# Kernel optimization log

Hardware: AMD Instinct MI355X
Metric: run time of the kernel (lower is better)

## Reference

```python
import jax, jax.numpy as jnp
import numpy as np

V = 256   # ascii_max_dim / output vocab
H = 1024  # h_size


def _lstm(x1h, W_ih, W_hh, b_ih, b_hh):
    """Single-layer unidirectional LSTM (PyTorch gate order i,f,g,o).
    x1h: [B,T,V] one-hot inputs; returns hidden states [B,T,H]."""
    B, T, _ = x1h.shape
    # input projection for all timesteps at once: [B,T,4H]
    xg = jnp.einsum('btv,gv->btg', x1h, W_ih) + b_ih + b_hh

    def step(carry, xt):
        h, c = carry
        gates = xt + h @ W_hh.T  # [B,4H]
        i, f, g, o = jnp.split(gates, 4, axis=-1)
        i = jax.nn.sigmoid(i)
        f = jax.nn.sigmoid(f)
        g = jnp.tanh(g)
        o = jax.nn.sigmoid(o)
        c = f * c + i * g
        h = o * jnp.tanh(c)
        return (h, c), h

    h0 = jnp.zeros((B, H), xg.dtype)
    c0 = jnp.zeros((B, H), xg.dtype)
    _, hs = jax.lax.scan(step, (h0, c0), jnp.swapaxes(xg, 0, 1))  # [T,B,H]
    return jnp.swapaxes(hs, 0, 1)  # [B,T,H]


def setup_inputs() -> dict:
    key = jax.random.key(0)
    ks = jax.random.split(key, 8)
    B, T = 8, 2048
    s = 0.05
    return {
        'Xs': jax.random.randint(ks[0], (B, T), 0, V),
        'ys': jax.random.randint(ks[1], (B, T), 0, V),
        'predict': 0,
        'W_ih': jax.random.normal(ks[2], (4 * H, V), dtype=jnp.float32) * s,
        'W_hh': jax.random.normal(ks[3], (4 * H, H), dtype=jnp.float32) * s,
        'b_ih': jax.random.normal(ks[4], (4 * H,), dtype=jnp.float32) * s,
        'b_hh': jax.random.normal(ks[5], (4 * H,), dtype=jnp.float32) * s,
        'W1': jax.random.normal(ks[6], (V, H), dtype=jnp.float32) * s,
        'b1': jax.random.normal(ks[7], (V,), dtype=jnp.float32) * s,
    }


def reference(Xs, ys, predict, W_ih, W_hh, b_ih, b_hh, W1, b1):
    # one-hot encode char ids -> [B,T,V]
    x1h = jax.nn.one_hot(Xs, V, dtype=W_ih.dtype)
    hs = _lstm(x1h, W_ih, W_hh, b_ih, b_hh)            # [B,T,H]
    logits = jnp.einsum('bth,vh->btv', hs, W1) + b1    # [B,T,V]
    if predict:
        prob = jax.nn.softmax(logits, axis=-1)
        return prob, jnp.argmax(prob, axis=-1)
    # CrossEntropyLoss (mean over timesteps) per sequence, averaged over sequences;
    # with equal lengths this is the mean NLL over all (B,T) positions.
    logp = jax.nn.log_softmax(logits, axis=-1)
    nll = -jnp.take_along_axis(logp, ys[..., None], axis=-1).squeeze(-1)
    return jnp.mean(nll)
```

## Files before the change

kernel.cpp:

```cpp
#include <hip/hip_runtime.h>

#define H_  1024
#define B_  8
#define T_  2048
#define V_  256
#define NWG 256
#define NTH 512
#define WPS (B_ * H_ / 4)

typedef unsigned long long u64;

__device__ __forceinline__ u64 agload64(const u64* p) {
  return __hip_atomic_load(p, __ATOMIC_RELAXED, __HIP_MEMORY_SCOPE_AGENT);
}
__device__ __forceinline__ void agstore64(u64* p, u64 v) {
  __hip_atomic_store(p, v, __ATOMIC_RELAXED, __HIP_MEMORY_SCOPE_AGENT);
}
__device__ __forceinline__ unsigned f2bf(float f) {
  unsigned u = __builtin_bit_cast(unsigned, f);
  return (u + 0x7fffu + ((u >> 16) & 1u)) >> 16;
}
__device__ __forceinline__ unsigned f2bf14(float f) {
  unsigned u = __builtin_bit_cast(unsigned, f);
  return ((u + 0x1FFFFu + ((u >> 18) & 1u)) >> 18) << 2;
}

__global__ __launch_bounds__(NTH, 1)
void charrnn_lstm(const int* __restrict__ Xs, const int* __restrict__ ys,
                  const float* __restrict__ W_ih, const float* __restrict__ W_hh,
                  const float* __restrict__ b_ih, const float* __restrict__ b_hh,
                  const float* __restrict__ W1, const float* __restrict__ b1,
                  float* __restrict__ out, u64* __restrict__ hg64)
{
  __shared__ float hstage[B_][H_];
  __shared__ float Wis[16][V_];
  __shared__ float stash[H_];
  __shared__ float logits_s[V_];
  __shared__ float gates_s[16][8];
  __shared__ float c_s[4][8];
  __shared__ float bias_s[16];
  __shared__ int   xw[8][32];

  const int wg   = blockIdx.x;
  const int tid  = threadIdx.x;
  const int b_g  = wg & 7;
  const int slot = wg >> 3;
  const int row  = tid >> 5;
  const int seg  = tid & 31;

  const int rg = (row >> 2) * H_ + wg * 4 + (row & 3);
  float4 wreg[8];
  #pragma unroll
  for (int q = 0; q < 8; ++q)
    wreg[q] = *(const float4*)&W_hh[(size_t)rg * H_ + seg * 4 + q * 128];

  for (int i = tid; i < 16 * (V_ / 4); i += NTH) {
    int rl = i >> 6;
    int kq = i & 63;
    int rr = (rl >> 2) * H_ + wg * 4 + (rl & 3);
    *(float4*)&Wis[rl][kq * 4] = *(const float4*)&W_ih[(size_t)rr * V_ + kq * 4];
  }
  if (tid < 16) {
    int rr = (tid >> 2) * H_ + wg * 4 + (tid & 3);
    bias_s[tid] = b_ih[rr] + b_hh[rr];
  }
  if (tid < 32) c_s[tid >> 3][tid & 7] = 0.f;

  int   pending = 0, chunk = 0, ptau = 0;
  float wg_loss = 0.f;

  auto do_chunk = [&]() {
    const int v_loc = tid >> 6, lane64 = tid & 63;
    const int vg = chunk * 8 + v_loc;
    const float* wrow = &W1[(size_t)vg * H_];
    float4 la = make_float4(0.f, 0.f, 0.f, 0.f);
    #pragma unroll
    for (int j = 0; j < 4; ++j) {
      const int k0 = lane64 * 4 + j * 256;
      const float4 w4 = *(const float4*)&wrow[k0];
      const float4 h4 = *(const float4*)&stash[k0];
      la.x = fmaf(w4.x, h4.x, la.x);
      la.y = fmaf(w4.y, h4.y, la.y);
      la.z = fmaf(w4.z, h4.z, la.z);
      la.w = fmaf(w4.w, h4.w, la.w);
    }
    float l = (la.x + la.y) + (la.z + la.w);
    #pragma unroll
    for (int m = 1; m < 64; m <<= 1) l += __shfl_xor(l, m, 64);
    if (lane64 == 0) logits_s[vg] = l + b1[vg];
    chunk++;
    if (chunk == 32) {
      __syncthreads();
      if (tid < 64) {
        float mx = -3.4e38f;
        #pragma unroll
        for (int i2 = 0; i2 < 4; ++i2) mx = fmaxf(mx, logits_s[tid * 4 + i2]);
        #pragma unroll
        for (int m = 1; m < 64; m <<= 1) mx = fmaxf(mx, __shfl_xor(mx, m, 64));
        float se = 0.f;
        #pragma unroll
        for (int i2 = 0; i2 < 4; ++i2) se += __expf(logits_s[tid * 4 + i2] - mx);
        #pragma unroll
        for (int m = 1; m < 64; m <<= 1) se += __shfl_xor(se, m, 64);
        if (tid == 0) {
          const float ly = logits_s[ys[b_g * T_ + ptau]];
          wg_loss += -(ly - mx - __logf(se));
        }
      }
      pending = 0;
      chunk = 0;
      __syncthreads();
    }
  };

  __syncthreads();

  for (int t = 0; t < T_; ++t) {
    const u64* hb = hg64 + (size_t)((t + 1) & 1) * WPS;
    const unsigned tagp = (unsigned)t & 3u;
    u64 v[4];
    for (;;) {
      bool ok = true;
      #pragma unroll
      for (int i = 0; i < 4; ++i) v[i] = agload64(&hb[i * NTH + tid]);
      #pragma unroll
      for (int i = 0; i < 4; ++i) ok &= (((unsigned)v[i] & 3u) == tagp);
      if (ok) break;
      __builtin_amdgcn_s_sleep(1);
    }
    #pragma unroll
    for (int i = 0; i < 4; ++i) {
      const int idx = i * NTH + tid;
      const int b = idx >> 8, u4 = idx & 255;
      const unsigned lo = (unsigned)v[i], hi = (unsigned)(v[i] >> 32);
      float4 f;
      f.x = __builtin_bit_cast(float, (lo & 0xFFFCu) << 16);
      f.y = __builtin_bit_cast(float, lo & 0xFFFF0000u);
      f.z = __builtin_bit_cast(float, (hi & 0xFFFFu) << 16);
      f.w = __builtin_bit_cast(float, hi & 0xFFFF0000u);
      *(float4*)&hstage[b][u4 * 4] = f;
    }
    if ((t & 31) == 0 && tid < 256) {
      const int b = tid >> 5, tt = t + (tid & 31);
      xw[b][tid & 31] = (tt < T_) ? Xs[b * T_ + tt] : 0;
    }
    __syncthreads();

    float4 acc[8];
    #pragma unroll
    for (int b = 0; b < 8; ++b) acc[b] = make_float4(0.f, 0.f, 0.f, 0.f);
    #pragma unroll
    for (int q = 0; q < 8; ++q) {
      const int k0 = seg * 4 + q * 128;
      const float4 w = wreg[q];
      #pragma unroll
      for (int b = 0; b < 8; ++b) {
        const float4 h4 = *(const float4*)&hstage[b][k0];
        acc[b].x = fmaf(w.x, h4.x, acc[b].x);
        acc[b].y = fmaf(w.y, h4.y, acc[b].y);
        acc[b].z = fmaf(w.z, h4.z, acc[b].z);
        acc[b].w = fmaf(w.w, h4.w, acc[b].w);
      }
    }
    float s[8];
    #pragma unroll
    for (int b = 0; b < 8; ++b) s[b] = (acc[b].x + acc[b].y) + (acc[b].z + acc[b].w);
    #pragma unroll
    for (int m = 1; m < 32; m <<= 1) {
      #pragma unroll
      for (int b = 0; b < 8; ++b) s[b] += __shfl_xor(s[b], m, 64);
    }
    if (seg < 8)
      gates_s[row][seg] = s[seg] + Wis[row][xw[seg][t & 31]] + bias_s[row];
    __syncthreads();

    if (tid < 32) {
      const int jj = tid >> 3, b = tid & 7;
      float iv = gates_s[jj][b],      fv = gates_s[4 + jj][b];
      float gv = gates_s[8 + jj][b],  ov = gates_s[12 + jj][b];
      iv = 1.f / (1.f + __expf(-iv));
      fv = 1.f / (1.f + __expf(-fv));
      gv = tanhf(gv);
      ov = 1.f / (1.f + __expf(-ov));
      const float c = fv * c_s[jj][b] + iv * gv;
      c_s[jj][b] = c;
      const float h = ov * tanhf(c);
      const unsigned full = f2bf(h);
      const unsigned tagd = f2bf14(h) | ((unsigned)(t + 1) & 3u);
      const unsigned r16 = (jj == 0) ? tagd : full;
      const unsigned p1 = (unsigned)__shfl((int)r16, b + 8, 64);
      const unsigned p2 = (unsigned)__shfl((int)r16, b + 16, 64);
      const unsigned p3 = (unsigned)__shfl((int)r16, b + 24, 64);
      if (tid < 8) {
        const u64 w = (u64)r16 | ((u64)p1 << 16) | ((u64)p2 << 32) | ((u64)p3 << 48);
        agstore64(&hg64[(size_t)(t & 1) * WPS + tid * 256 + wg], w);
      }
    }

    const int tau = t - 1;
    const bool newst = (tau >= 0 && (tau & 31) == slot && !pending);
    if (newst) {
      for (int i = tid; i < H_; i += NTH) stash[i] = hstage[b_g][i];
    }
    if (newst) { pending = 1; chunk = 0; ptau = tau; }
    __syncthreads();

    if (pending) do_chunk();
  }

  while (pending) do_chunk();

  if (slot == 31) {
    const u64* hb = hg64 + (size_t)((T_ - 1) & 1) * WPS;
    if (tid < 256) {
      u64 w;
      do { w = agload64(&hb[b_g * 256 + tid]); }
      while (((unsigned)w & 3u) != ((unsigned)T_ & 3u));
      const unsigned lo = (unsigned)w, hi = (unsigned)(w >> 32);
      float4 f;
      f.x = __builtin_bit_cast(float, (lo & 0xFFFCu) << 16);
      f.y = __builtin_bit_cast(float, lo & 0xFFFF0000u);
      f.z = __builtin_bit_cast(float, (hi & 0xFFFFu) << 16);
      f.w = __builtin_bit_cast(float, hi & 0xFFFF0000u);
      *(float4*)&stash[tid * 4] = f;
    }
    pending = 1; chunk = 0; ptau = T_ - 1;
    __syncthreads();
    while (pending) do_chunk();
  }

  if (tid == 0) atomicAdd(out, wg_loss * (1.0f / (B_ * T_)));
}

extern "C" void kernel_launch(void* const* d_in, const int* in_sizes, int n_in,
                              void* d_out, int out_size, void* d_ws, size_t ws_size,
                              hipStream_t stream) {
  const int*   Xs   = (const int*)d_in[0];
  const int*   ys   = (const int*)d_in[1];
  const float* W_ih = (const float*)d_in[3];
  const float* W_hh = (const float*)d_in[4];
  const float* b_ih = (const float*)d_in[5];
  const float* b_hh = (const float*)d_in[6];
  const float* W1   = (const float*)d_in[7];
  const float* b1   = (const float*)d_in[8];
  float* out = (float*)d_out;

  u64* hg64 = (u64*)d_ws;

  hipMemsetAsync(d_out, 0, sizeof(float) * (size_t)out_size, stream);
  hipMemsetAsync(d_ws, 0, 2 * WPS * sizeof(u64), stream);

  void* args[] = { (void*)&Xs, (void*)&ys, (void*)&W_ih, (void*)&W_hh,
                   (void*)&b_ih, (void*)&b_hh, (void*)&W1, (void*)&b1,
                   (void*)&out, (void*)&hg64 };
  hipError_t e = hipLaunchCooperativeKernel((const void*)charrnn_lstm, dim3(NWG),
                                            dim3(NTH), args, 0, stream);
  if (e != hipSuccess) {
    hipLaunchKernelGGL(charrnn_lstm, dim3(NWG), dim3(NTH), 0, stream,
                       Xs, ys, W_ih, W_hh, b_ih, b_hh, W1, b1, out, hg64);
  }
}
```

Baseline: 8.746 ms.

## Partition LSTM by batch element with per-group sync and bf16 register weights

Each workgroup now owns one batch element and 32 hidden units (128 gate rows) instead of 4 units across all batch elements. Each group of 32 workgroups exchanges hidden state through its own small buffer, so every step polls only 256 words. The recurrent weights are packed as bf16 pairs into 128 registers per thread, and the input projection is gathered per step from W_ih instead of being staged in shared memory. The aim is less global polling and synchronisation fan-in per step, at the cost of reduced weight precision and heavy register pressure under launch_bounds(512,2), which may cause spills.

```diff
diff --git a/kernel.cpp b/kernel.cpp
--- a/kernel.cpp
+++ b/kernel.cpp
@@ -6,9 +6,12 @@
 #define V_  256
 #define NWG 256
 #define NTH 512
-#define WPS (B_ * H_ / 4)
+#define NGRP 8
+#define NRANK 32
+#define WPG 256
 
 typedef unsigned long long u64;
+typedef unsigned u32;
 
 __device__ __forceinline__ u64 agload64(const u64* p) {
   return __hip_atomic_load(p, __ATOMIC_RELAXED, __HIP_MEMORY_SCOPE_AGENT);
@@ -16,55 +19,58 @@
 __device__ __forceinline__ void agstore64(u64* p, u64 v) {
   __hip_atomic_store(p, v, __ATOMIC_RELAXED, __HIP_MEMORY_SCOPE_AGENT);
 }
-__device__ __forceinline__ unsigned f2bf(float f) {
-  unsigned u = __builtin_bit_cast(unsigned, f);
+__device__ __forceinline__ u32 f2bf(float f) {
+  u32 u = __builtin_bit_cast(u32, f);
   return (u + 0x7fffu + ((u >> 16) & 1u)) >> 16;
 }
-__device__ __forceinline__ unsigned f2bf14(float f) {
-  unsigned u = __builtin_bit_cast(unsigned, f);
+__device__ __forceinline__ u32 f2bf14(float f) {
+  u32 u = __builtin_bit_cast(u32, f);
   return ((u + 0x1FFFFu + ((u >> 18) & 1u)) >> 18) << 2;
 }
-
-__global__ __launch_bounds__(NTH, 1)
+__device__ __forceinline__ float bflo(u32 w) {
+  return __builtin_bit_cast(float, w << 16);
+}
+__device__ __forceinline__ float bfhi(u32 w) {
+  return __builtin_bit_cast(float, w & 0xFFFF0000u);
+}
+
+__global__ __launch_bounds__(NTH, 2)
 void charrnn_lstm(const int* __restrict__ Xs, const int* __restrict__ ys,
                   const float* __restrict__ W_ih, const float* __restrict__ W_hh,
                   const float* __restrict__ b_ih, const float* __restrict__ b_hh,
                   const float* __restrict__ W1, const float* __restrict__ b1,
                   float* __restrict__ out, u64* __restrict__ hg64)
 {
-  __shared__ float hstage[B_][H_];
-  __shared__ float Wis[16][V_];
+  __shared__ float hstage[4 * 264];
   __shared__ float stash[H_];
   __shared__ float logits_s[V_];
-  __shared__ float gates_s[16][8];
-  __shared__ float c_s[4][8];
-  __shared__ float bias_s[16];
-  __shared__ int   xw[8][32];
+  __shared__ float gates_s[128];
+  __shared__ float c_s[NRANK];
 
   const int wg   = blockIdx.x;
   const int tid  = threadIdx.x;
-  const int b_g  = wg & 7;
-  const int slot = wg >> 3;
-  const int row  = tid >> 5;
-  const int seg  = tid & 31;
-
-  const int rg = (row >> 2) * H_ + wg * 4 + (row & 3);
-  float4 wreg[8];
+  const int g    = wg & 7;
+  const int rank = wg >> 3;
+  const int slot = rank;
+  const int r_loc = tid >> 2;
+  const int seg   = tid & 3;
+  const int g4    = r_loc >> 5;
+  const int u_loc = r_loc & 31;
+  const int rg    = g4 * H_ + rank * NRANK + u_loc;
+
+  u64* gbuf = hg64 + (size_t)g * (2 * WPG);
+
+  u32 wp[128];
   #pragma unroll
-  for (int q = 0; q < 8; ++q)
-    wreg[q] = *(const float4*)&W_hh[(size_t)rg * H_ + seg * 4 + q * 128];
-
-  for (int i = tid; i < 16 * (V_ / 4); i += NTH) {
-    int rl = i >> 6;
-    int kq = i & 63;
-    int rr = (rl >> 2) * H_ + wg * 4 + (rl & 3);
-    *(float4*)&Wis[rl][kq * 4] = *(const float4*)&W_ih[(size_t)rr * V_ + kq * 4];
-  }
-  if (tid < 16) {
-    int rr = (tid >> 2) * H_ + wg * 4 + (tid & 3);
-    bias_s[tid] = b_ih[rr] + b_hh[rr];
-  }
-  if (tid < 32) c_s[tid >> 3][tid & 7] = 0.f;
+  for (int q = 0; q < 64; ++q) {
+    const float4 w4 = *(const float4*)&W_hh[(size_t)rg * H_ + seg * 256 + q * 4];
+    wp[2 * q]     = f2bf(w4.x) | (f2bf(w4.y) << 16);
+    wp[2 * q + 1] = f2bf(w4.z) | (f2bf(w4.w) << 16);
+  }
+  const float breg = b_ih[rg] + b_hh[rg];
+  if (tid < NRANK) c_s[tid] = 0.f;
+
+  float xv = W_ih[(size_t)rg * V_ + Xs[g * T_]];
 
   int   pending = 0, chunk = 0, ptau = 0;
   float wg_loss = 0.f;
@@ -103,7 +109,7 @@
         #pragma unroll
         for (int m = 1; m < 64; m <<= 1) se += __shfl_xor(se, m, 64);
         if (tid == 0) {
-          const float ly = logits_s[ys[b_g * T_ + ptau]];
+          const float ly = logits_s[ys[g * T_ + ptau]];
           wg_loss += -(ly - mx - __logf(se));
         }
       }
@@ -116,91 +122,71 @@
   __syncthreads();
 
   for (int t = 0; t < T_; ++t) {
-    const u64* hb = hg64 + (size_t)((t + 1) & 1) * WPS;
-    const unsigned tagp = (unsigned)t & 3u;
-    u64 v[4];
-    for (;;) {
-      bool ok = true;
-      #pragma unroll
-      for (int i = 0; i < 4; ++i) v[i] = agload64(&hb[i * NTH + tid]);
-      #pragma unroll
-      for (int i = 0; i < 4; ++i) ok &= (((unsigned)v[i] & 3u) == tagp);
-      if (ok) break;
-      __builtin_amdgcn_s_sleep(1);
-    }
-    #pragma unroll
-    for (int i = 0; i < 4; ++i) {
-      const int idx = i * NTH + tid;
-      const int b = idx >> 8, u4 = idx & 255;
-      const unsigned lo = (unsigned)v[i], hi = (unsigned)(v[i] >> 32);
+    const u64* hb = gbuf + ((t + 1) & 1) * WPG;
+    const u32 tagp = (u32)t & 3u;
+    if (tid < WPG) {
+      u64 v;
+      do { v = agload64(&hb[tid]); } while (((u32)v & 3u) != tagp);
+      const u32 lo = (u32)v, hi = (u32)(v >> 32);
       float4 f;
       f.x = __builtin_bit_cast(float, (lo & 0xFFFCu) << 16);
       f.y = __builtin_bit_cast(float, lo & 0xFFFF0000u);
       f.z = __builtin_bit_cast(float, (hi & 0xFFFFu) << 16);
       f.w = __builtin_bit_cast(float, hi & 0xFFFF0000u);
-      *(float4*)&hstage[b][u4 * 4] = f;
-    }
-    if ((t & 31) == 0 && tid < 256) {
-      const int b = tid >> 5, tt = t + (tid & 31);
-      xw[b][tid & 31] = (tt < T_) ? Xs[b * T_ + tt] : 0;
-    }
-    __syncthreads();
-
-    float4 acc[8];
+      *(float4*)&hstage[(tid >> 6) * 264 + ((4 * tid) & 255)] = f;
+    }
+    const int cnext = Xs[g * T_ + ((t + 1 < T_) ? t + 1 : T_ - 1)];
+    const float xv_next = W_ih[(size_t)rg * V_ + cnext];
+    __syncthreads();
+
+    const float* hseg = &hstage[seg * 264];
+    float a0 = 0.f, a1 = 0.f;
     #pragma unroll
-    for (int b = 0; b < 8; ++b) acc[b] = make_float4(0.f, 0.f, 0.f, 0.f);
-    #pragma unroll
-    for (int q = 0; q < 8; ++q) {
-      const int k0 = seg * 4 + q * 128;
-      const float4 w = wreg[q];
-      #pragma unroll
-      for (int b = 0; b < 8; ++b) {
-        const float4 h4 = *(const float4*)&hstage[b][k0];
-        acc[b].x = fmaf(w.x, h4.x, acc[b].x);
-        acc[b].y = fmaf(w.y, h4.y, acc[b].y);
-        acc[b].z = fmaf(w.z, h4.z, acc[b].z);
-        acc[b].w = fmaf(w.w, h4.w, acc[b].w);
-      }
-    }
-    float s[8];
-    #pragma unroll
-    for (int b = 0; b < 8; ++b) s[b] = (acc[b].x + acc[b].y) + (acc[b].z + acc[b].w);
-    #pragma unroll
-    for (int m = 1; m < 32; m <<= 1) {
-      #pragma unroll
-      for (int b = 0; b < 8; ++b) s[b] += __shfl_xor(s[b], m, 64);
-    }
-    if (seg < 8)
-      gates_s[row][seg] = s[seg] + Wis[row][xw[seg][t & 31]] + bias_s[row];
-    __syncthreads();
-
-    if (tid < 32) {
-      const int jj = tid >> 3, b = tid & 7;
-      float iv = gates_s[jj][b],      fv = gates_s[4 + jj][b];
-      float gv = gates_s[8 + jj][b],  ov = gates_s[12 + jj][b];
+    for (int q = 0; q < 64; ++q) {
+      const float4 h4 = *(const float4*)&hseg[q * 4];
+      const u32 wa = wp[2 * q], wb = wp[2 * q + 1];
+      a0 = fmaf(bflo(wa), h4.x, a0);
+      a1 = fmaf(bfhi(wa), h4.y, a1);
+      a0 = fmaf(bflo(wb), h4.z, a0);
+      a1 = fmaf(bfhi(wb), h4.w, a1);
+    }
+    float p = a0 + a1;
+    p += __shfl_xor(p, 1, 64);
+    p += __shfl_xor(p, 2, 64);
+    if (seg == 0) gates_s[r_loc] = p + xv + breg;
+    __syncthreads();
+
+    if (tid < NRANK) {
+      const int u = tid;
+      float iv = gates_s[u],      fv = gates_s[32 + u];
+      float gv = gates_s[64 + u], ov = gates_s[96 + u];
       iv = 1.f / (1.f + __expf(-iv));
       fv = 1.f / (1.f + __expf(-fv));
       gv = tanhf(gv);
       ov = 1.f / (1.f + __expf(-ov));
-      const float c = fv * c_s[jj][b] + iv * gv;
-      c_s[jj][b] = c;
+      const float c = fv * c_s[u] + iv * gv;
+      c_s[u] = c;
       const float h = ov * tanhf(c);
-      const unsigned full = f2bf(h);
-      const unsigned tagd = f2bf14(h) | ((unsigned)(t + 1) & 3u);
-      const unsigned r16 = (jj == 0) ? tagd : full;
-      const unsigned p1 = (unsigned)__shfl((int)r16, b + 8, 64);
-      const unsigned p2 = (unsigned)__shfl((int)r16, b + 16, 64);
-      const unsigned p3 = (unsigned)__shfl((int)r16, b + 24, 64);
+      const u32 full = f2bf(h);
+      const u32 tagd = f2bf14(h) | ((u32)(t + 1) & 3u);
+      const u32 r16 = ((u & 3) == 0) ? tagd : full;
+      const u32 v0 = (u32)__shfl((int)r16, 4 * tid,     64);
+      const u32 v1 = (u32)__shfl((int)r16, 4 * tid + 1, 64);
+      const u32 v2 = (u32)__shfl((int)r16, 4 * tid + 2, 64);
+      const u32 v3 = (u32)__shfl((int)r16, 4 * tid + 3, 64);
       if (tid < 8) {
-        const u64 w = (u64)r16 | ((u64)p1 << 16) | ((u64)p2 << 32) | ((u64)p3 << 48);
-        agstore64(&hg64[(size_t)(t & 1) * WPS + tid * 256 + wg], w);
+        const u64 w = (u64)v0 | ((u64)v1 << 16) | ((u64)v2 << 32) | ((u64)v3 << 48);
+        agstore64(&gbuf[(t & 1) * WPG + rank * 8 + tid], w);
       }
     }
+    xv = xv_next;
 
     const int tau = t - 1;
     const bool newst = (tau >= 0 && (tau & 31) == slot && !pending);
     if (newst) {
-      for (int i = tid; i < H_; i += NTH) stash[i] = hstage[b_g][i];
+      const int i0 = tid, i1 = tid + 512;
+      stash[i0] = hstage[(i0 >> 8) * 264 + (i0 & 255)];
+      stash[i1] = hstage[(i1 >> 8) * 264 + (i1 & 255)];
     }
     if (newst) { pending = 1; chunk = 0; ptau = tau; }
     __syncthreads();
@@ -211,18 +197,17 @@
   while (pending) do_chunk();
 
   if (slot == 31) {
-    const u64* hb = hg64 + (size_t)((T_ - 1) & 1) * WPS;
-    if (tid < 256) {
-      u64 w;
-      do { w = agload64(&hb[b_g * 256 + tid]); }
-      while (((unsigned)w & 3u) != ((unsigned)T_ & 3u));
-      const unsigned lo = (unsigned)w, hi = (unsigned)(w >> 32);
+    const u64* hb = gbuf + ((T_ - 1) & 1) * WPG;
+    if (tid < WPG) {
+      u64 v;
+      do { v = agload64(&hb[tid]); } while (((u32)v & 3u) != ((u32)T_ & 3u));
+      const u32 lo = (u32)v, hi = (u32)(v >> 32);
       float4 f;
       f.x = __builtin_bit_cast(float, (lo & 0xFFFCu) << 16);
       f.y = __builtin_bit_cast(float, lo & 0xFFFF0000u);
       f.z = __builtin_bit_cast(float, (hi & 0xFFFFu) << 16);
       f.w = __builtin_bit_cast(float, hi & 0xFFFF0000u);
-      *(float4*)&stash[tid * 4] = f;
+      *(float4*)&stash[4 * tid] = f;
     }
     pending = 1; chunk = 0; ptau = T_ - 1;
     __syncthreads();
@@ -248,7 +233,7 @@
   u64* hg64 = (u64*)d_ws;
 
   hipMemsetAsync(d_out, 0, sizeof(float) * (size_t)out_size, stream);
-  hipMemsetAsync(d_ws, 0, 2 * WPS * sizeof(u64), stream);
+  hipMemsetAsync(d_ws, 0, NGRP * 2 * WPG * sizeof(u64), stream);
 
   void* args[] = { (void*)&Xs, (void*)&ys, (void*)&W_ih, (void*)&W_hh,
                    (void*)&b_ih, (void*)&b_hh, (void*)&W1, (void*)&b1,
```

Result: slower. 30.30 ms (+246.5%).

## Move output projection and loss out of recurrent loop into separate kernels

Applied to the files above, without the earlier changes.

The recurrent kernel now only computes the LSTM. Each workgroup writes its assigned timestep's packed bf16 hidden state to a global buffer instead of computing logits and softmax in chunks interleaved with the recurrence. A separate loss kernel, one block per timestep, computes logits for all 8 batches at once, reusing each W1 row across the batch. A reduce kernel then sums the per-timestep partial losses. This shortens the serial per-step critical path, which previously carried an extra barrier and the chunked W1 work, at the cost of two extra launches and a global round trip for the hidden states.

```diff
diff --git a/kernel.cpp b/kernel.cpp
--- a/kernel.cpp
+++ b/kernel.cpp
@@ -8,7 +8,12 @@
 #define NTH 512
 #define WPS (B_ * H_ / 4)
 
+#define OFF_TRANS 0u
+#define OFF_PART  (64u << 10)
+#define OFF_HS    (1u << 20)
+
 typedef unsigned long long u64;
+typedef unsigned u32;
 
 __device__ __forceinline__ u64 agload64(const u64* p) {
   return __hip_atomic_load(p, __ATOMIC_RELAXED, __HIP_MEMORY_SCOPE_AGENT);
@@ -16,26 +21,33 @@
 __device__ __forceinline__ void agstore64(u64* p, u64 v) {
   __hip_atomic_store(p, v, __ATOMIC_RELAXED, __HIP_MEMORY_SCOPE_AGENT);
 }
-__device__ __forceinline__ unsigned f2bf(float f) {
-  unsigned u = __builtin_bit_cast(unsigned, f);
+__device__ __forceinline__ u32 f2bf(float f) {
+  u32 u = __builtin_bit_cast(u32, f);
   return (u + 0x7fffu + ((u >> 16) & 1u)) >> 16;
 }
-__device__ __forceinline__ unsigned f2bf14(float f) {
-  unsigned u = __builtin_bit_cast(unsigned, f);
+__device__ __forceinline__ u32 f2bf14(float f) {
+  u32 u = __builtin_bit_cast(u32, f);
   return ((u + 0x1FFFFu + ((u >> 18) & 1u)) >> 18) << 2;
 }
 
+__device__ __forceinline__ float4 dec4(u64 v) {
+  const u32 lo = (u32)v, hi = (u32)(v >> 32);
+  float4 f;
+  f.x = __builtin_bit_cast(float, (lo & 0xFFFCu) << 16);
+  f.y = __builtin_bit_cast(float, lo & 0xFFFF0000u);
+  f.z = __builtin_bit_cast(float, (hi & 0xFFFFu) << 16);
+  f.w = __builtin_bit_cast(float, hi & 0xFFFF0000u);
+  return f;
+}
+
 __global__ __launch_bounds__(NTH, 1)
-void charrnn_lstm(const int* __restrict__ Xs, const int* __restrict__ ys,
-                  const float* __restrict__ W_ih, const float* __restrict__ W_hh,
-                  const float* __restrict__ b_ih, const float* __restrict__ b_hh,
-                  const float* __restrict__ W1, const float* __restrict__ b1,
-                  float* __restrict__ out, u64* __restrict__ hg64)
+void charrnn_lstm(const int* __restrict__ Xs, const float* __restrict__ W_ih,
+                  const float* __restrict__ W_hh, const float* __restrict__ b_ih,
+                  const float* __restrict__ b_hh, u64* __restrict__ hg64,
+                  u64* __restrict__ hs)
 {
   __shared__ float hstage[B_][H_];
   __shared__ float Wis[16][V_];
-  __shared__ float stash[H_];
-  __shared__ float logits_s[V_];
   __shared__ float gates_s[16][8];
   __shared__ float c_s[4][8];
   __shared__ float bias_s[16];
@@ -65,80 +77,28 @@
     bias_s[tid] = b_ih[rr] + b_hh[rr];
   }
   if (tid < 32) c_s[tid >> 3][tid & 7] = 0.f;
-
-  int   pending = 0, chunk = 0, ptau = 0;
-  float wg_loss = 0.f;
-
-  auto do_chunk = [&]() {
-    const int v_loc = tid >> 6, lane64 = tid & 63;
-    const int vg = chunk * 8 + v_loc;
-    const float* wrow = &W1[(size_t)vg * H_];
-    float4 la = make_float4(0.f, 0.f, 0.f, 0.f);
-    #pragma unroll
-    for (int j = 0; j < 4; ++j) {
-      const int k0 = lane64 * 4 + j * 256;
-      const float4 w4 = *(const float4*)&wrow[k0];
-      const float4 h4 = *(const float4*)&stash[k0];
-      la.x = fmaf(w4.x, h4.x, la.x);
-      la.y = fmaf(w4.y, h4.y, la.y);
-      la.z = fmaf(w4.z, h4.z, la.z);
-      la.w = fmaf(w4.w, h4.w, la.w);
-    }
-    float l = (la.x + la.y) + (la.z + la.w);
-    #pragma unroll
-    for (int m = 1; m < 64; m <<= 1) l += __shfl_xor(l, m, 64);
-    if (lane64 == 0) logits_s[vg] = l + b1[vg];
-    chunk++;
-    if (chunk == 32) {
-      __syncthreads();
-      if (tid < 64) {
-        float mx = -3.4e38f;
-        #pragma unroll
-        for (int i2 = 0; i2 < 4; ++i2) mx = fmaxf(mx, logits_s[tid * 4 + i2]);
-        #pragma unroll
-        for (int m = 1; m < 64; m <<= 1) mx = fmaxf(mx, __shfl_xor(mx, m, 64));
-        float se = 0.f;
-        #pragma unroll
-        for (int i2 = 0; i2 < 4; ++i2) se += __expf(logits_s[tid * 4 + i2] - mx);
-        #pragma unroll
-        for (int m = 1; m < 64; m <<= 1) se += __shfl_xor(se, m, 64);
-        if (tid == 0) {
-          const float ly = logits_s[ys[b_g * T_ + ptau]];
-          wg_loss += -(ly - mx - __logf(se));
-        }
-      }
-      pending = 0;
-      chunk = 0;
-      __syncthreads();
-    }
-  };
-
   __syncthreads();
 
   for (int t = 0; t < T_; ++t) {
     const u64* hb = hg64 + (size_t)((t + 1) & 1) * WPS;
-    const unsigned tagp = (unsigned)t & 3u;
+    const u32 tagp = (u32)t & 3u;
     u64 v[4];
     for (;;) {
       bool ok = true;
       #pragma unroll
       for (int i = 0; i < 4; ++i) v[i] = agload64(&hb[i * NTH + tid]);
       #pragma unroll
-      for (int i = 0; i < 4; ++i) ok &= (((unsigned)v[i] & 3u) == tagp);
+      for (int i = 0; i < 4; ++i) ok &= (((u32)v[i] & 3u) == tagp);
       if (ok) break;
       __builtin_amdgcn_s_sleep(1);
     }
+    if (t > 0 && ((t - 1) & 31) == slot && (tid >> 8) == (b_g & 1))
+      hs[((size_t)(t - 1) * B_ + b_g) * 256 + (tid & 255)] = v[b_g >> 1];
     #pragma unroll
     for (int i = 0; i < 4; ++i) {
       const int idx = i * NTH + tid;
       const int b = idx >> 8, u4 = idx & 255;
-      const unsigned lo = (unsigned)v[i], hi = (unsigned)(v[i] >> 32);
-      float4 f;
-      f.x = __builtin_bit_cast(float, (lo & 0xFFFCu) << 16);
-      f.y = __builtin_bit_cast(float, lo & 0xFFFF0000u);
-      f.z = __builtin_bit_cast(float, (hi & 0xFFFFu) << 16);
-      f.w = __builtin_bit_cast(float, hi & 0xFFFF0000u);
-      *(float4*)&hstage[b][u4 * 4] = f;
+      *(float4*)&hstage[b][u4 * 4] = dec4(v[i]);
     }
     if ((t & 31) == 0 && tid < 256) {
       const int b = tid >> 5, tt = t + (tid & 31);
@@ -185,51 +145,101 @@
       const float c = fv * c_s[jj][b] + iv * gv;
       c_s[jj][b] = c;
       const float h = ov * tanhf(c);
-      const unsigned full = f2bf(h);
-      const unsigned tagd = f2bf14(h) | ((unsigned)(t + 1) & 3u);
-      const unsigned r16 = (jj == 0) ? tagd : full;
-      const unsigned p1 = (unsigned)__shfl((int)r16, b + 8, 64);
-      const unsigned p2 = (unsigned)__shfl((int)r16, b + 16, 64);
-      const unsigned p3 = (unsigned)__shfl((int)r16, b + 24, 64);
+      const u32 full = f2bf(h);
+      const u32 tagd = f2bf14(h) | ((u32)(t + 1) & 3u);
+      const u32 r16 = ((jj & 3) == 0) ? tagd : full;
+      const u32 p1 = (u32)__shfl((int)r16, b + 8, 64);
+      const u32 p2 = (u32)__shfl((int)r16, b + 16, 64);
+      const u32 p3 = (u32)__shfl((int)r16, b + 24, 64);
       if (tid < 8) {
         const u64 w = (u64)r16 | ((u64)p1 << 16) | ((u64)p2 << 32) | ((u64)p3 << 48);
         agstore64(&hg64[(size_t)(t & 1) * WPS + tid * 256 + wg], w);
       }
     }
-
-    const int tau = t - 1;
-    const bool newst = (tau >= 0 && (tau & 31) == slot && !pending);
-    if (newst) {
-      for (int i = tid; i < H_; i += NTH) stash[i] = hstage[b_g][i];
-    }
-    if (newst) { pending = 1; chunk = 0; ptau = tau; }
-    __syncthreads();
-
-    if (pending) do_chunk();
-  }
-
-  while (pending) do_chunk();
-
-  if (slot == 31) {
-    const u64* hb = hg64 + (size_t)((T_ - 1) & 1) * WPS;
-    if (tid < 256) {
-      u64 w;
-      do { w = agload64(&hb[b_g * 256 + tid]); }
-      while (((unsigned)w & 3u) != ((unsigned)T_ & 3u));
-      const unsigned lo = (unsigned)w, hi = (unsigned)(w >> 32);
-      float4 f;
-      f.x = __builtin_bit_cast(float, (lo & 0xFFFCu) << 16);
-      f.y = __builtin_bit_cast(float, lo & 0xFFFF0000u);
-      f.z = __builtin_bit_cast(float, (hi & 0xFFFFu) << 16);
-      f.w = __builtin_bit_cast(float, hi & 0xFFFF0000u);
-      *(float4*)&stash[tid * 4] = f;
-    }
-    pending = 1; chunk = 0; ptau = T_ - 1;
-    __syncthreads();
-    while (pending) do_chunk();
-  }
-
-  if (tid == 0) atomicAdd(out, wg_loss * (1.0f / (B_ * T_)));
+  }
+
+  if (slot == 31 && (tid >> 8) == (b_g & 1)) {
+    const u64* hb = hg64 + (size_t)((T_ + 1) & 1) * WPS;
+    const int idx = (b_g >> 1) * NTH + tid;
+    u64 v = agload64(&hb[idx]);
+    while (((u32)v & 3u) != ((u32)T_ & 3u)) {
+      __builtin_amdgcn_s_sleep(1);
+      v = agload64(&hb[idx]);
+    }
+    hs[((size_t)(T_ - 1) * B_ + b_g) * 256 + (tid & 255)] = v;
+  }
+}
+
+__global__ __launch_bounds__(256, 4)
+void loss_kernel(const int* __restrict__ ys, const float* __restrict__ b1,
+                 const float* __restrict__ W1, const u64* __restrict__ hs,
+                 float* __restrict__ partials) {
+  __shared__ float hs_s[B_][H_];
+  __shared__ float logits_s[B_][V_];
+  const int tau = blockIdx.x;
+  const int tid = threadIdx.x;
+
+  #pragma unroll
+  for (int b = 0; b < B_; ++b)
+    *(float4*)&hs_s[b][tid * 4] = dec4(hs[((size_t)tau * B_ + b) * 256 + tid]);
+  __syncthreads();
+
+  const float* wrow = &W1[(size_t)tid * H_];
+  float4 a[B_];
+  #pragma unroll
+  for (int b = 0; b < B_; ++b) a[b] = make_float4(0.f, 0.f, 0.f, 0.f);
+  #pragma unroll 4
+  for (int k = 0; k < 256; ++k) {
+    const float4 w4 = *(const float4*)&wrow[k * 4];
+    #pragma unroll
+    for (int b = 0; b < B_; ++b) {
+      const float4 h4 = *(const float4*)&hs_s[b][k * 4];
+      a[b].x = fmaf(w4.x, h4.x, a[b].x);
+      a[b].y = fmaf(w4.y, h4.y, a[b].y);
+      a[b].z = fmaf(w4.z, h4.z, a[b].z);
+      a[b].w = fmaf(w4.w, h4.w, a[b].w);
+    }
+  }
+  const float bb = b1[tid];
+  #pragma unroll
+  for (int b = 0; b < B_; ++b)
+    logits_s[b][tid] = (a[b].x + a[b].y) + (a[b].z + a[b].w) + bb;
+  __syncthreads();
+
+  const int wv = tid >> 6, lane = tid & 63;
+  float acc = 0.f;
+  #pragma unroll
+  for (int h = 0; h < 2; ++h) {
+    const int b = wv + h * 4;
+    const float* lg = logits_s[b];
+    float mx = fmaxf(fmaxf(lg[lane * 4], lg[lane * 4 + 1]),
+                     fmaxf(lg[lane * 4 + 2], lg[lane * 4 + 3]));
+    #pragma unroll
+    for (int m = 1; m < 64; m <<= 1) mx = fmaxf(mx, __shfl_xor(mx, m, 64));
+    float se = __expf(lg[lane * 4] - mx) + __expf(lg[lane * 4 + 1] - mx) +
+               __expf(lg[lane * 4 + 2] - mx) + __expf(lg[lane * 4 + 3] - mx);
+    #pragma unroll
+    for (int m = 1; m < 64; m <<= 1) se += __shfl_xor(se, m, 64);
+    if (lane == 0) acc += -(lg[ys[b * T_ + tau]] - mx - __logf(se));
+  }
+  __shared__ float pacc[4];
+  if (lane == 0) pacc[wv] = acc;
+  __syncthreads();
+  if (tid == 0) partials[tau] = (pacc[0] + pacc[1]) + (pacc[2] + pacc[3]);
+}
+
+__global__ __launch_bounds__(256, 1)
+void reduce_kernel(const float* __restrict__ partials, float* __restrict__ out) {
+  const int tid = threadIdx.x;
+  float acc = 0.f;
+  #pragma unroll
+  for (int i = 0; i < T_ / 256; ++i) acc += partials[i * 256 + tid];
+  #pragma unroll
+  for (int m = 1; m < 64; m <<= 1) acc += __shfl_xor(acc, m, 64);
+  __shared__ float w[4];
+  if ((tid & 63) == 0) w[tid >> 6] = acc;
+  __syncthreads();
+  if (tid == 0) out[0] = ((w[0] + w[1]) + (w[2] + w[3])) * (1.0f / (B_ * T_));
 }
 
 extern "C" void kernel_launch(void* const* d_in, const int* in_sizes, int n_in,
@@ -245,18 +255,21 @@
   const float* b1   = (const float*)d_in[8];
   float* out = (float*)d_out;
 
-  u64* hg64 = (u64*)d_ws;
-
-  hipMemsetAsync(d_out, 0, sizeof(float) * (size_t)out_size, stream);
-  hipMemsetAsync(d_ws, 0, 2 * WPS * sizeof(u64), stream);
-
-  void* args[] = { (void*)&Xs, (void*)&ys, (void*)&W_ih, (void*)&W_hh,
-                   (void*)&b_ih, (void*)&b_hh, (void*)&W1, (void*)&b1,
-                   (void*)&out, (void*)&hg64 };
+  u64*   hg64     = (u64*)((char*)d_ws + OFF_TRANS);
+  float* partials = (float*)((char*)d_ws + OFF_PART);
+  u64*   hs       = (u64*)((char*)d_ws + OFF_HS);
+
+  hipMemsetAsync(hg64, 0, 2 * WPS * sizeof(u64), stream);
+
+  void* args[] = { (void*)&Xs, (void*)&W_ih, (void*)&W_hh, (void*)&b_ih,
+                   (void*)&b_hh, (void*)&hg64, (void*)&hs };
   hipError_t e = hipLaunchCooperativeKernel((const void*)charrnn_lstm, dim3(NWG),
                                             dim3(NTH), args, 0, stream);
   if (e != hipSuccess) {
     hipLaunchKernelGGL(charrnn_lstm, dim3(NWG), dim3(NTH), 0, stream,
-                       Xs, ys, W_ih, W_hh, b_ih, b_hh, W1, b1, out, hg64);
-  }
-}
+                       Xs, W_ih, W_hh, b_ih, b_hh, hg64, hs);
+  }
+
+  loss_kernel<<<T_, 256, 0, stream>>>(ys, b1, W1, hs, partials);
+  reduce_kernel<<<1, 256, 0, stream>>>(partials, out);
+}
```

After: 16.35 ms. 87.0% more time.
